# Performance work log

Hardware: AMD Instinct MI355X
Metric: run time of the kernel (lower is better)

## Reference

```python
import jax, jax.numpy as jnp
import numpy as np

# Sizes (must match input_specs)
N_CHR, E_CHR = 50000, 500000
N_SLV, E_SLV = 30000, 300000
B = 256            # number of graphs in the batch
FEAT = 64          # num_node_feats
DIM = 128          # hidden dim
HALF = DIM // 2    # last GCN layer output
ENS = 3            # ensemble per branch type


def setup_inputs() -> dict:
    key = jax.random.key(0)
    ks = jax.random.split(key, 20)
    g = lambda k, shape, fan_in: jax.random.normal(k, shape, dtype=jnp.float32) / np.sqrt(fan_in)
    inp = {
        'chr_x': jax.random.normal(ks[0], (N_CHR, FEAT), dtype=jnp.float32),
        'slv_x': jax.random.normal(ks[1], (N_SLV, FEAT), dtype=jnp.float32),
        'chr_edge_index': jax.random.randint(ks[2], (2, E_CHR), 0, N_CHR),
        'slv_edge_index': jax.random.randint(ks[3], (2, E_SLV), 0, N_SLV),
        'chr_x_batch': jnp.sort(jax.random.randint(ks[4], (N_CHR,), 0, B)),
        'slv_x_batch': jnp.sort(jax.random.randint(ks[5], (N_SLV,), 0, B)),
        # GCN weights, stacked over ensemble (GCNConv: bias=False)
        'chr_W0': g(ks[6], (ENS, FEAT, DIM), FEAT),
        'chr_W1': g(ks[7], (ENS, DIM, DIM), DIM),
        'chr_W2': g(ks[8], (ENS, DIM, HALF), DIM),
        'slv_W0': g(ks[9], (ENS, FEAT, DIM), FEAT),
        'slv_W1': g(ks[10], (ENS, DIM, DIM), DIM),
        'slv_W2': g(ks[11], (ENS, DIM, HALF), DIM),
        # per-ensemble projection heads (nn.Linear with bias)
        'cfc_W': g(ks[12], (ENS, HALF, DIM), HALF),
        'cfc_b': jnp.zeros((ENS, DIM), dtype=jnp.float32),
        'sfc_W': g(ks[13], (ENS, HALF, DIM), HALF),
        'sfc_b': jnp.zeros((ENS, DIM), dtype=jnp.float32),
        # final MLP head
        'fc1_W': g(ks[14], (2 * ENS * DIM, DIM), 2 * ENS * DIM),
        'fc1_b': jnp.zeros((DIM,), dtype=jnp.float32),
        'fc2_W': g(ks[15], (DIM, 1), DIM),
        'fc2_b': jnp.zeros((1,), dtype=jnp.float32),
    }
    return inp


def _gcn(x, W, src, dst, n_nodes):
    # GCNConv(normalize=False, bias=False, aggr='add'):
    # out[i] = sum_{(j,i) in E} (x @ W)[j]   (no self-loops, no normalization)
    h = x @ W
    return jax.ops.segment_sum(h[src], dst, num_segments=n_nodes)


def _branch(x, W0, W1, W2, edge_index, batch_ids, n_nodes):
    src, dst = edge_index[0], edge_index[1]
    h = jax.nn.relu(_gcn(x, W0, src, dst, n_nodes))
    h = jax.nn.relu(_gcn(h, W1, src, dst, n_nodes))
    h = jax.nn.relu(_gcn(h, W2, src, dst, n_nodes))
    # global_add_pool
    return jax.ops.segment_sum(h, batch_ids, num_segments=B)  # [B, HALF]


def reference(chr_x, slv_x, chr_W0, chr_W1, chr_W2, slv_W0, slv_W1, slv_W2,
              cfc_W, cfc_b, sfc_W, sfc_b, fc1_W, fc1_b, fc2_W, fc2_b,
              chr_edge_index, slv_edge_index, chr_x_batch, slv_x_batch):
    # vmap over the ensemble dimension (independent GCN stacks share inputs)
    rep_chr = jax.vmap(lambda w0, w1, w2: _branch(chr_x, w0, w1, w2, chr_edge_index, chr_x_batch, N_CHR))(
        chr_W0, chr_W1, chr_W2)  # [ENS, B, HALF]
    rep_slv = jax.vmap(lambda w0, w1, w2: _branch(slv_x, w0, w1, w2, slv_edge_index, slv_x_batch, N_SLV))(
        slv_W0, slv_W1, slv_W2)  # [ENS, B, HALF]
    ind_chr = jax.nn.relu(jnp.einsum('ebd,edh->ebh', rep_chr, cfc_W) + cfc_b[:, None, :])  # [ENS, B, DIM]
    ind_slv = jax.nn.relu(jnp.einsum('ebd,edh->ebh', rep_slv, sfc_W) + sfc_b[:, None, :])
    # torch.cat(ind_chr + ind_slv, dim=1): chr branches first, then slv branches
    hg = jnp.concatenate([
        jnp.transpose(ind_chr, (1, 0, 2)).reshape(B, ENS * DIM),
        jnp.transpose(ind_slv, (1, 0, 2)).reshape(B, ENS * DIM)], axis=1)  # [B, 2*ENS*DIM]
    hg = jax.nn.relu(hg @ fc1_W + fc1_b)
    out = hg @ fc2_W + fc2_b  # [B, 1]
    return out
```

## Files before the change

### kernel.cpp

```cpp
#include <hip/hip_runtime.h>

#define N_CHR 50000
#define E_CHR 500000
#define N_SLV 30000
#define E_SLV 300000
#define E_TOT (E_CHR + E_SLV)
#define BATCH_B 256
#define FEAT 64
#define DIM 128
#define HALF 64
#define ENSN 3
#define CB_CHR ((N_CHR + 255) / 256)
#define CB_SLV ((N_SLV + 255) / 256)
#define CB_TOT (CB_CHR + CB_SLV)
#define NBLK 128
#define SLOTS (NBLK * 4)
#define CHUNK ((E_TOT + NBLK - 1) / NBLK)

typedef unsigned int u32;
typedef unsigned short u16;
typedef __attribute__((ext_vector_type(8))) short short8;
typedef __attribute__((ext_vector_type(4))) float floatx4;
typedef __attribute__((ext_vector_type(4))) unsigned int u32x4;


__device__ inline u16 f2b(float f) {
    u32 u = __builtin_bit_cast(u32, f);
    u += 0x7FFFu + ((u >> 16) & 1u);
    return (u16)(u >> 16);
}
__device__ inline float b2f_lo(u32 v) { return __builtin_bit_cast(float, v << 16); }
__device__ inline float b2f_hi(u32 v) { return __builtin_bit_cast(float, v & 0xFFFF0000u); }
__device__ inline u32 packb(float a, float b) { return (u32)f2b(a) | ((u32)f2b(b) << 16); }

__device__ inline void acc8(float* a, u32x4 v) {
    a[0] += b2f_lo(v.x); a[1] += b2f_hi(v.x);
    a[2] += b2f_lo(v.y); a[3] += b2f_hi(v.y);
    a[4] += b2f_lo(v.z); a[5] += b2f_hi(v.z);
    a[6] += b2f_lo(v.w); a[7] += b2f_hi(v.w);
}


__global__ void xconv_k(const float* __restrict__ xc, const float* __restrict__ xs,
                        u16* __restrict__ oc, u16* __restrict__ os) {
    const int nc = N_CHR * FEAT, ns = N_SLV * FEAT;
    int i = blockIdx.x * blockDim.x + threadIdx.x;
    int stride = gridDim.x * blockDim.x;
    for (; i < nc + ns; i += stride) {
        if (i < nc) oc[i] = f2b(xc[i]);
        else os[i - nc] = f2b(xs[i - nc]);
    }
}


__global__ void wconv6_k(const float* __restrict__ cW0, const float* __restrict__ cW1,
                         const float* __restrict__ cW2, const float* __restrict__ sW0,
                         const float* __restrict__ sW1, const float* __restrict__ sW2,
                         u16* __restrict__ cW0t, u16* __restrict__ cW1t, u16* __restrict__ cW2t,
                         u16* __restrict__ sW0t, u16* __restrict__ sW1t, u16* __restrict__ sW2t) {
    int z = blockIdx.z, e = blockIdx.y;
    const float* W; u16* Wt; int K, N;
    switch (z) {
        case 0: W = cW0; Wt = cW0t; K = FEAT; N = DIM;  break;
        case 1: W = cW1; Wt = cW1t; K = DIM;  N = DIM;  break;
        case 2: W = cW2; Wt = cW2t; K = DIM;  N = HALF; break;
        case 3: W = sW0; Wt = sW0t; K = FEAT; N = DIM;  break;
        case 4: W = sW1; Wt = sW1t; K = DIM;  N = DIM;  break;
        default: W = sW2; Wt = sW2t; K = DIM; N = HALF; break;
    }
    int idx = blockIdx.x * 256 + threadIdx.x;
    if (idx >= K * N) return;
    int k = idx / N, nn = idx - k * N;
    Wt[((size_t)e * N + nn) * K + k] = f2b(W[(size_t)e * K * N + idx]);
}


__global__ __launch_bounds__(256) void hist_blocks_k(
        const int* __restrict__ cdst, const int* __restrict__ sdst,
        int* __restrict__ gh, int* __restrict__ btot) {
    __shared__ int h[4][CB_TOT];
    int blk = blockIdx.x, t = threadIdx.x, wv = t >> 6;
    for (int i = t; i < 4 * CB_TOT; i += 256) ((int*)h)[i] = 0;
    __syncthreads();
    int s = blk * CHUNK, e = s + CHUNK;
    if (e > E_TOT) e = E_TOT;
    for (int i = s + t; i < e; i += 256) {
        int bkt = (i < E_CHR) ? (cdst[i] >> 8) : (CB_CHR + (sdst[i - E_CHR] >> 8));
        atomicAdd(&h[wv][bkt], 1);
    }
    __syncthreads();
    for (int j = t; j < CB_TOT; j += 256) {
        int s0 = h[0][j], s1 = h[1][j], s2 = h[2][j], s3 = h[3][j];
        gh[j * SLOTS + blk * 4 + 0] = s0;
        gh[j * SLOTS + blk * 4 + 1] = s1;
        gh[j * SLOTS + blk * 4 + 2] = s2;
        gh[j * SLOTS + blk * 4 + 3] = s3;
        int tot = s0 + s1 + s2 + s3;
        if (tot) atomicAdd(&btot[j], tot);
    }
}

__global__ void coarse_scan_k(const int* __restrict__ cnt, int* __restrict__ off) {
    int t = threadIdx.x;
    const int PER = (CB_TOT + 63) / 64;
    int loc[PER];
    int sum = 0;
    int s = t * PER;
#pragma unroll
    for (int k = 0; k < PER; k++) {
        int i = s + k;
        int v = (i < CB_TOT) ? cnt[i] : 0;
        loc[k] = sum;
        sum += v;
    }
    int inc = sum;
#pragma unroll
    for (int o = 1; o < 64; o <<= 1) {
        int sh = __shfl_up(inc, o, 64);
        if (t >= o) inc += sh;
    }
    int pre = inc - sum;
#pragma unroll
    for (int k = 0; k < PER; k++) {
        int i = s + k;
        if (i < CB_TOT) off[i] = pre + loc[k];
    }
    if (t == 63) off[CB_TOT] = inc;
}

__device__ inline int block_exscan(int v) {
    int lane = threadIdx.x & 63, wv = threadIdx.x >> 6;
    int inc = v;
#pragma unroll
    for (int o = 1; o < 64; o <<= 1) {
        int t = __shfl_up(inc, o, 64);
        if (lane >= o) inc += t;
    }
    __shared__ int ws[4];
    if (lane == 63) ws[wv] = inc;
    __syncthreads();
    if (threadIdx.x == 0) {
        int c = 0;
#pragma unroll
        for (int k = 0; k < 4; k++) { int t = ws[k]; ws[k] = c; c += t; }
    }
    __syncthreads();
    int r = ws[wv] + inc - v;
    __syncthreads();
    return r;
}

__global__ __launch_bounds__(256) void block_base_k(int* __restrict__ gh,
                                                    const int* __restrict__ coff) {
    int j = blockIdx.x, t = threadIdx.x;
    int v0 = gh[j * SLOTS + 2 * t], v1 = gh[j * SLOTS + 2 * t + 1];
    int p = block_exscan(v0 + v1);
    gh[j * SLOTS + 2 * t] = coff[j] + p;
    gh[j * SLOTS + 2 * t + 1] = coff[j] + p + v0;
}

__global__ __launch_bounds__(256) void scatter2_k(
        const int* __restrict__ cei, const int* __restrict__ sei,
        const int* __restrict__ gh, u32* __restrict__ staging) {
    __shared__ int cur[4][CB_TOT];
    int blk = blockIdx.x, t = threadIdx.x, wv = t >> 6;
    for (int i = t; i < 4 * CB_TOT; i += 256) {
        int w = i / CB_TOT, j = i - w * CB_TOT;
        ((int*)cur)[i] = gh[j * SLOTS + blk * 4 + w];
    }
    __syncthreads();
    int s = blk * CHUNK, e = s + CHUNK;
    if (e > E_TOT) e = E_TOT;
    for (int i = s + t; i < e; i += 256) {
        int src, dst, bkt;
        if (i < E_CHR) {
            src = cei[i]; dst = cei[E_CHR + i]; bkt = dst >> 8;
        } else {
            int j2 = i - E_CHR;
            src = sei[j2]; dst = sei[E_SLV + j2]; bkt = CB_CHR + (dst >> 8);
        }
        int p = atomicAdd(&cur[wv][bkt], 1);
        staging[p] = (u32)src | ((u32)(dst & 255) << 17);
    }
}

__global__ __launch_bounds__(256) void bucket_sort_k(
        const u32* __restrict__ staging, const int* __restrict__ coff,
        int* __restrict__ off_c, int* __restrict__ off_s,
        int* __restrict__ csr_c, int* __restrict__ csr_s) {
    int b = blockIdx.x, t = threadIdx.x, wv = t >> 6;
    int isS = b >= CB_CHR;
    int base = coff[b], end = coff[b + 1];
    int n = isS ? N_SLV : N_CHR;
    int* off = isS ? off_s : off_c;
    int* csr = isS ? csr_s : csr_c;
    int outBase = isS ? base - E_CHR : base;
    int nodeBase = (isS ? (b - CB_CHR) : b) << 8;
    __shared__ int h4[4][256];
    __shared__ int cur[256];
    h4[0][t] = 0; h4[1][t] = 0; h4[2][t] = 0; h4[3][t] = 0;
    __syncthreads();
    for (int i = base + t; i < end; i += 256)
        atomicAdd(&h4[wv][staging[i] >> 17], 1);
    __syncthreads();
    int tot = h4[0][t] + h4[1][t] + h4[2][t] + h4[3][t];
    int p = block_exscan(tot);
    int node = nodeBase + t;
    if (node <= n) off[node] = outBase + p;
    cur[t] = p;
    __syncthreads();
    for (int i = base + t; i < end; i += 256) {
        u32 v = staging[i];
        int pos = atomicAdd(&cur[v >> 17], 1);
        csr[outBase + pos] = (int)(v & 0x1FFFFu);
    }
}


__global__ __launch_bounds__(256) void agg1gemm_k(
        const u16* __restrict__ Xc, const int* __restrict__ offc, const int* __restrict__ csrc,
        const u16* __restrict__ W0c, u16* __restrict__ Yc, int nc,
        const u16* __restrict__ Xs, const int* __restrict__ offs, const int* __restrict__ csrs,
        const u16* __restrict__ W0s, u16* __restrict__ Ys, int ns) {
    __shared__ u32x4 at4[64 * 8];
    __shared__ u32x4 wt4[128 * 8];
    int z = blockIdx.z;
    int n = z ? ns : nc;
    const int* off = z ? offs : offc;
    const int* csr = z ? csrs : csrc;
    const u32x4* X4 = (const u32x4*)(z ? Xs : Xc);
    const u16* W0 = z ? W0s : W0c;
    u16* Y = z ? Ys : Yc;
    int i0 = blockIdx.x * 64;
    if (i0 >= n) return;
    int t = threadIdx.x;
    int nl = t >> 2, c0 = t & 3;
    int i = i0 + nl;
    float a[16] = {0,0,0,0,0,0,0,0,0,0,0,0,0,0,0,0};
    if (i < n) {
        int s = off[i], e2 = off[i + 1], j = s;
        for (; j + 1 < e2; j += 2) {
            size_t r0 = (size_t)csr[j] * 8, r1 = (size_t)csr[j + 1] * 8;
            u32x4 v0 = X4[r0 + c0], v1 = X4[r0 + c0 + 4];
            u32x4 w0 = X4[r1 + c0], w1 = X4[r1 + c0 + 4];
            acc8(a, v0); acc8(a + 8, v1); acc8(a, w0); acc8(a + 8, w1);
        }
        if (j < e2) {
            size_t r0 = (size_t)csr[j] * 8;
            acc8(a, X4[r0 + c0]); acc8(a + 8, X4[r0 + c0 + 4]);
        }
    }
    u32x4 o0, o1;
    o0.x = packb(a[0], a[1]);  o0.y = packb(a[2], a[3]);
    o0.z = packb(a[4], a[5]);  o0.w = packb(a[6], a[7]);
    o1.x = packb(a[8], a[9]);  o1.y = packb(a[10], a[11]);
    o1.z = packb(a[12], a[13]); o1.w = packb(a[14], a[15]);
    int sw = nl & 7;
    at4[nl * 8 + (c0 ^ sw)] = o0;
    at4[nl * 8 + ((c0 + 4) ^ sw)] = o1;
    int wave = t >> 6, lane = t & 63, quad = lane >> 4, nq = lane & 15;
    int arow = wave * 16 + nq;
    for (int e = 0; e < ENSN; e++) {
        __syncthreads();
        const u16* We = W0 + (size_t)e * DIM * FEAT;
        for (int ci = t; ci < 128 * 8; ci += 256) {
            int row = ci >> 3, c = ci & 7;
            wt4[row * 8 + (c ^ (row & 7))] = *(const u32x4*)(We + (size_t)row * FEAT + c * 8);
        }
        __syncthreads();
        floatx4 acc[8];
#pragma unroll
        for (int tt = 0; tt < 8; tt++) acc[tt] = (floatx4)(0.f);
#pragma unroll
        for (int kt = 0; kt < 2; kt++) {
            int ck = kt * 4 + quad;
            short8 af = *(const short8*)&at4[arow * 8 + (ck ^ (arow & 7))];
#pragma unroll
            for (int tt = 0; tt < 8; tt++) {
                int br = tt * 16 + nq;
                short8 bf = *(const short8*)&wt4[br * 8 + (ck ^ (br & 7))];
                acc[tt] = __builtin_amdgcn_mfma_f32_16x16x32_bf16(af, bf, acc[tt], 0, 0, 0);
            }
        }
        u16* Ye = Y + (size_t)e * (size_t)n * DIM;
#pragma unroll
        for (int tt = 0; tt < 8; tt++)
#pragma unroll
            for (int r = 0; r < 4; r++) {
                int row = i0 + wave * 16 + quad * 4 + r;
                if (row < n) Ye[(size_t)row * DIM + tt * 16 + nq] = f2b(fmaxf(acc[tt][r], 0.f));
            }
    }
}


__global__ __launch_bounds__(256) void aggb128cs_k(
        const u16* __restrict__ Hc, const int* __restrict__ offc, const int* __restrict__ csrc,
        u16* __restrict__ Yc, int nc,
        const u16* __restrict__ Hs, const int* __restrict__ offs, const int* __restrict__ csrs,
        u16* __restrict__ Ys, int ns) {
    int z = blockIdx.z;
    int n = z ? ns : nc;
    const int* off = z ? offs : offc;
    const int* csr = z ? csrs : csrc;
    int e = blockIdx.y >> 1, ch = blockIdx.y & 1;
    const u32x4* He = (const u32x4*)((z ? Hs : Hc) + (size_t)e * n * DIM);
    u32x4* Ye = (u32x4*)((z ? Ys : Yc) + (size_t)e * n * DIM);
    int i = blockIdx.x * 32 + (threadIdx.x >> 3);
    if (i >= n) return;
    int l8 = (threadIdx.x & 7) + ch * 8;
    int s = off[i], e2 = off[i + 1];
    float a[8] = {0.f, 0.f, 0.f, 0.f, 0.f, 0.f, 0.f, 0.f};
    int j = s;
    for (; j + 3 < e2; j += 4) {
        u32x4 v0 = He[(size_t)csr[j] * 16 + l8];
        u32x4 v1 = He[(size_t)csr[j + 1] * 16 + l8];
        u32x4 v2 = He[(size_t)csr[j + 2] * 16 + l8];
        u32x4 v3 = He[(size_t)csr[j + 3] * 16 + l8];
        acc8(a, v0); acc8(a, v1); acc8(a, v2); acc8(a, v3);
    }
    for (; j < e2; j++) acc8(a, He[(size_t)csr[j] * 16 + l8]);
    u32x4 o;
    o.x = packb(a[0], a[1]); o.y = packb(a[2], a[3]);
    o.z = packb(a[4], a[5]); o.w = packb(a[6], a[7]);
    Ye[(size_t)i * 16 + l8] = o;
}


__global__ __launch_bounds__(256) void gemm23_k(
        const u16* __restrict__ Xc, const u16* __restrict__ W1c, const u16* __restrict__ W2c,
        u16* __restrict__ Yc, int nc,
        const u16* __restrict__ Xs, const u16* __restrict__ W1s, const u16* __restrict__ W2s,
        u16* __restrict__ Ys, int ns) {
    __shared__ u16 wlds[DIM * DIM];
    __shared__ u16 hlds[4 * 32 * DIM];
    const int z = blockIdx.z, e = blockIdx.y;
    const int n = z ? ns : nc;
    const u16* Xe = (z ? Xs : Xc) + (size_t)e * (size_t)n * DIM;
    const u16* W1 = (z ? W1s : W1c) + (size_t)e * DIM * DIM;
    const u16* W2 = (z ? W2s : W2c) + (size_t)e * HALF * DIM;
    u16* Ye = (z ? Ys : Yc) + (size_t)e * (size_t)n * HALF;
    for (int c = threadIdx.x; c < DIM * (DIM / 8); c += 256) {
        int row = c >> 4, seg = c & 15;
        *(short8*)(wlds + row * DIM + ((seg ^ (row & 15)) << 3)) =
            *(const short8*)(W1 + (size_t)row * DIM + (seg << 3));
    }
    __syncthreads();
    int wave = threadIdx.x >> 6, lane = threadIdx.x & 63;
    int quad = lane >> 4, nq = lane & 15;
    int m0 = blockIdx.x * 128 + wave * 32;
    floatx4 acc[2][8];
#pragma unroll
    for (int rg = 0; rg < 2; rg++)
#pragma unroll
        for (int t = 0; t < 8; t++) acc[rg][t] = (floatx4)(0.f);
#pragma unroll
    for (int kt = 0; kt < 4; kt++) {
        int k0 = kt * 32 + quad * 8;
        short8 a[2];
#pragma unroll
        for (int rg = 0; rg < 2; rg++) {
            int row = m0 + rg * 16 + nq;
            int rc = row < n ? row : (n - 1);
            a[rg] = *(const short8*)(Xe + (size_t)rc * DIM + k0);
        }
#pragma unroll
        for (int t = 0; t < 8; t++) {
            int rb = t * 16 + nq;
            short8 b = *(const short8*)(wlds + rb * DIM + ((((kt << 2) + quad) ^ nq) << 3));
#pragma unroll
            for (int rg = 0; rg < 2; rg++)
                acc[rg][t] = __builtin_amdgcn_mfma_f32_16x16x32_bf16(a[rg], b, acc[rg][t], 0, 0, 0);
        }
    }
    u16* hw = hlds + wave * 32 * DIM;
#pragma unroll
    for (int rg = 0; rg < 2; rg++)
#pragma unroll
        for (int t = 0; t < 8; t++)
#pragma unroll
            for (int r = 0; r < 4; r++) {
                int rl = rg * 16 + quad * 4 + r;
                int col = t * 16 + nq;
                hw[rl * DIM + (((col >> 3) ^ (rl & 15)) << 3) + (col & 7)] =
                    f2b(fmaxf(acc[rg][t][r], 0.f));
            }
    __syncthreads();
    for (int c = threadIdx.x; c < HALF * (DIM / 8); c += 256) {
        int row = c >> 4, seg = c & 15;
        *(short8*)(wlds + row * DIM + ((seg ^ (row & 15)) << 3)) =
            *(const short8*)(W2 + (size_t)row * DIM + (seg << 3));
    }
    __syncthreads();
    floatx4 acc2[2][4];
#pragma unroll
    for (int rg = 0; rg < 2; rg++)
#pragma unroll
        for (int t = 0; t < 4; t++) acc2[rg][t] = (floatx4)(0.f);
#pragma unroll
    for (int kt = 0; kt < 4; kt++) {
        int k0q = (kt << 2) + quad;
        short8 a[2];
#pragma unroll
        for (int rg = 0; rg < 2; rg++) {
            int rl = rg * 16 + nq;
            a[rg] = *(const short8*)(hw + rl * DIM + ((k0q ^ (rl & 15)) << 3));
        }
#pragma unroll
        for (int t = 0; t < 4; t++) {
            int rb = t * 16 + nq;
            short8 b = *(const short8*)(wlds + rb * DIM + ((k0q ^ nq) << 3));
#pragma unroll
            for (int rg = 0; rg < 2; rg++)
                acc2[rg][t] = __builtin_amdgcn_mfma_f32_16x16x32_bf16(a[rg], b, acc2[rg][t], 0, 0, 0);
        }
    }
#pragma unroll
    for (int rg = 0; rg < 2; rg++)
#pragma unroll
        for (int t = 0; t < 4; t++)
#pragma unroll
            for (int r = 0; r < 4; r++) {
                int row = m0 + rg * 16 + quad * 4 + r;
                if (row < n) Ye[(size_t)row * HALF + t * 16 + nq] = f2b(acc2[rg][t][r]);
            }
}


__global__ __launch_bounds__(256) void agg64poole_k(
        const u16* __restrict__ Pc, const int* __restrict__ offc, const int* __restrict__ csrc,
        const int* __restrict__ batc, int nc,
        const u16* __restrict__ Ps, const int* __restrict__ offs, const int* __restrict__ csrs,
        const int* __restrict__ bats, int ns,
        float* __restrict__ rep) {
    int z = blockIdx.z;
    int n = z ? ns : nc;
    const int* off = z ? offs : offc;
    const int* csr = z ? csrs : csrc;
    const int* batch = z ? bats : batc;
    const u16* P = z ? Ps : Pc;
    const u32x4* P0 = (const u32x4*)P;
    const u32x4* P1 = (const u32x4*)(P + (size_t)n * HALF);
    const u32x4* P2 = (const u32x4*)(P + 2 * (size_t)n * HALF);
    int i0 = blockIdx.x * 32;
    int nl = threadIdx.x >> 3, l8 = threadIdx.x & 7;
    int i = i0 + nl;
    float a0[8] = {0,0,0,0,0,0,0,0}, a1[8] = {0,0,0,0,0,0,0,0}, a2[8] = {0,0,0,0,0,0,0,0};
    if (i < n) {
        int s = off[i], e2 = off[i + 1];
        int j = s;
        for (; j + 1 < e2; j += 2) {
            size_t r0 = (size_t)csr[j] * 8 + l8, r1 = (size_t)csr[j + 1] * 8 + l8;
            u32x4 p0 = P0[r0], p1 = P1[r0], p2 = P2[r0];
            u32x4 q0 = P0[r1], q1 = P1[r1], q2 = P2[r1];
            acc8(a0, p0); acc8(a1, p1); acc8(a2, p2);
            acc8(a0, q0); acc8(a1, q1); acc8(a2, q2);
        }
        if (j < e2) {
            size_t r0 = (size_t)csr[j] * 8 + l8;
            acc8(a0, P0[r0]); acc8(a1, P1[r0]); acc8(a2, P2[r0]);
        }
    }
    __shared__ float sm[ENSN][32][64];
    __shared__ int gb[32];
#pragma unroll
    for (int k = 0; k < 8; k++) {
        sm[0][nl][l8 * 8 + k] = fmaxf(a0[k], 0.f);
        sm[1][nl][l8 * 8 + k] = fmaxf(a1[k], 0.f);
        sm[2][nl][l8 * 8 + k] = fmaxf(a2[k], 0.f);
    }
    if (threadIdx.x < 32) gb[threadIdx.x] = (i0 + (int)threadIdx.x < n) ? batch[i0 + threadIdx.x] : -1;
    __syncthreads();
    if (threadIdx.x < 192) {
        int e = threadIdx.x >> 6, f = threadIdx.x & 63;
        int colbase = z * (ENSN * HALF) + e * HALF + f;
        float acc = 0.f;
        int g = -2;
        for (int k = 0; k < 32; k++) {
            int gg = gb[k];
            if (gg != g) {
                if (g >= 0) atomicAdd(&rep[g * (2 * ENSN * HALF) + colbase], acc);
                acc = 0.f;
                g = gg;
            }
            if (gg >= 0) acc += sm[e][k][f];
        }
        if (g >= 0) atomicAdd(&rep[g * (2 * ENSN * HALF) + colbase], acc);
    }
}


__global__ __launch_bounds__(256) void headfinal_k(
        const float* __restrict__ rep,
        const float* __restrict__ cW, const float* __restrict__ cB,
        const float* __restrict__ sW, const float* __restrict__ sB,
        const float* __restrict__ W1, const float* __restrict__ b1,
        const float* __restrict__ W2, const float* __restrict__ b2,
        float* __restrict__ out) {
    int b = blockIdx.x, t = threadIdx.x;
    __shared__ float r[2 * ENSN * HALF];
    __shared__ float hg[2 * ENSN * DIM];
    __shared__ float red[DIM];
    for (int i = t; i < 2 * ENSN * HALF; i += 256) r[i] = rep[b * (2 * ENSN * HALF) + i];
    __syncthreads();
    for (int o = t; o < 2 * ENSN * DIM; o += 256) {
        int head = o >> 7, c = o & 127;
        int branch = head / ENSN, e = head - branch * ENSN;
        const float* W = (branch ? sW : cW) + (size_t)e * HALF * DIM;
        const float* rr = r + branch * (ENSN * HALF) + e * HALF;
        float acc = (branch ? sB : cB)[e * DIM + c];
#pragma unroll
        for (int k = 0; k < HALF; k++) acc = fmaf(rr[k], W[k * DIM + c], acc);
        hg[o] = fmaxf(acc, 0.f);
    }
    __syncthreads();
    if (t < DIM) {
        float acc = b1[t];
        for (int k = 0; k < 2 * ENSN * DIM; k++) acc = fmaf(hg[k], W1[k * DIM + t], acc);
        red[t] = fmaxf(acc, 0.f) * W2[t];
    }
    __syncthreads();
    if (t < 64) {
        float v = red[t] + red[t + 64];
#pragma unroll
        for (int o = 32; o > 0; o >>= 1) v += __shfl_down(v, o, 64);
        if (t == 0) out[b] = v + b2[0];
    }
}


extern "C" void kernel_launch(void* const* d_in, const int* in_sizes, int n_in,
                              void* d_out, int out_size, void* d_ws, size_t ws_size,
                              hipStream_t stream) {
    const float* chr_x = (const float*)d_in[0];
    const float* slv_x = (const float*)d_in[1];
    const int* chr_ei = (const int*)d_in[2];
    const int* slv_ei = (const int*)d_in[3];
    const int* chr_batch = (const int*)d_in[4];
    const int* slv_batch = (const int*)d_in[5];
    const float* chr_W0 = (const float*)d_in[6];
    const float* chr_W1 = (const float*)d_in[7];
    const float* chr_W2 = (const float*)d_in[8];
    const float* slv_W0 = (const float*)d_in[9];
    const float* slv_W1 = (const float*)d_in[10];
    const float* slv_W2 = (const float*)d_in[11];
    const float* cfc_W = (const float*)d_in[12];
    const float* cfc_b = (const float*)d_in[13];
    const float* sfc_W = (const float*)d_in[14];
    const float* sfc_b = (const float*)d_in[15];
    const float* fc1_W = (const float*)d_in[16];
    const float* fc1_b = (const float*)d_in[17];
    const float* fc2_W = (const float*)d_in[18];
    const float* fc2_b = (const float*)d_in[19];
    float* out = (float*)d_out;

    char* w = (char*)d_ws;
    auto carve = [&](size_t bytes) {
        void* p = (void*)w;
        w += (bytes + 255) & ~(size_t)255;
        return p;
    };
    int* off_chr = (int*)carve((N_CHR + 1) * sizeof(int));
    int* csr_chr = (int*)carve((size_t)E_CHR * sizeof(int));
    int* off_slv = (int*)carve((N_SLV + 1) * sizeof(int));
    int* csr_slv = (int*)carve((size_t)E_SLV * sizeof(int));
    int* btot    = (int*)carve(CB_TOT * sizeof(int));
    int* coff    = (int*)carve((CB_TOT + 1) * sizeof(int));
    int* gh      = (int*)carve((size_t)CB_TOT * SLOTS * sizeof(int));
    u32* staging = (u32*)carve((size_t)E_TOT * sizeof(u32));
    u16* cW0t = (u16*)carve((size_t)ENSN * DIM * FEAT * sizeof(u16));
    u16* cW1t = (u16*)carve((size_t)ENSN * DIM * DIM * sizeof(u16));
    u16* cW2t = (u16*)carve((size_t)ENSN * HALF * DIM * sizeof(u16));
    u16* sW0t = (u16*)carve((size_t)ENSN * DIM * FEAT * sizeof(u16));
    u16* sW1t = (u16*)carve((size_t)ENSN * DIM * DIM * sizeof(u16));
    u16* sW2t = (u16*)carve((size_t)ENSN * HALF * DIM * sizeof(u16));
    u16* xb_chr = (u16*)carve((size_t)N_CHR * FEAT * sizeof(u16));
    u16* xb_slv = (u16*)carve((size_t)N_SLV * FEAT * sizeof(u16));
    float* rep = (float*)carve((size_t)BATCH_B * 2 * ENSN * HALF * sizeof(float));
    u16* bufP_c = (u16*)carve((size_t)ENSN * N_CHR * DIM * sizeof(u16));
    u16* bufQ_c = (u16*)carve((size_t)ENSN * N_CHR * DIM * sizeof(u16));
    u16* bufP_s = (u16*)carve((size_t)ENSN * N_SLV * DIM * sizeof(u16));
    u16* bufQ_s = (u16*)carve((size_t)ENSN * N_SLV * DIM * sizeof(u16));

    xconv_k<<<512, 256, 0, stream>>>(chr_x, slv_x, xb_chr, xb_slv);
    wconv6_k<<<dim3(64, ENSN, 6), 256, 0, stream>>>(chr_W0, chr_W1, chr_W2,
                                                    slv_W0, slv_W1, slv_W2,
                                                    cW0t, cW1t, cW2t, sW0t, sW1t, sW2t);

    hipMemsetAsync(btot, 0, CB_TOT * sizeof(int), stream);
    hist_blocks_k<<<NBLK, 256, 0, stream>>>(chr_ei + E_CHR, slv_ei + E_SLV, gh, btot);
    coarse_scan_k<<<1, 64, 0, stream>>>(btot, coff);
    block_base_k<<<CB_TOT, 256, 0, stream>>>(gh, coff);
    scatter2_k<<<NBLK, 256, 0, stream>>>(chr_ei, slv_ei, gh, staging);
    bucket_sort_k<<<CB_TOT, 256, 0, stream>>>(staging, coff, off_chr, off_slv, csr_chr, csr_slv);

    hipMemsetAsync(rep, 0, (size_t)BATCH_B * 2 * ENSN * HALF * sizeof(float), stream);

    agg1gemm_k<<<dim3((N_CHR + 63) / 64, 1, 2), 256, 0, stream>>>(
        xb_chr, off_chr, csr_chr, cW0t, bufP_c, N_CHR,
        xb_slv, off_slv, csr_slv, sW0t, bufP_s, N_SLV);
    aggb128cs_k<<<dim3((N_CHR + 31) / 32, ENSN * 2, 2), 256, 0, stream>>>(
        bufP_c, off_chr, csr_chr, bufQ_c, N_CHR,
        bufP_s, off_slv, csr_slv, bufQ_s, N_SLV);
    gemm23_k<<<dim3((N_CHR + 127) / 128, ENSN, 2), 256, 0, stream>>>(
        bufQ_c, cW1t, cW2t, bufP_c, N_CHR,
        bufQ_s, sW1t, sW2t, bufP_s, N_SLV);
    agg64poole_k<<<dim3((N_CHR + 31) / 32, 1, 2), 256, 0, stream>>>(
        bufP_c, off_chr, csr_chr, chr_batch, N_CHR,
        bufP_s, off_slv, csr_slv, slv_batch, N_SLV, rep);

    headfinal_k<<<BATCH_B, 256, 0, stream>>>(rep, cfc_W, cfc_b, sfc_W, sfc_b,
                                             fc1_W, fc1_b, fc2_W, fc2_b, out);
}
```

Before: 373.5 us.

## Fuse layer-2 aggregation into GEMM23, fold memsets into kernels, split pool by ensemble

The layer-2 neighbor aggregation now runs inside the GEMM kernel. Each lane gathers and accumulates its rows' neighbor features into registers, and those registers become the MFMA A operands. This removes the write and re-read of the aggregated buffer and one launch. The two memsets move into existing kernels (xconv zeroes btot, hist zeroes rep), and the layer-3 pool kernel gains a grid dimension over the ensemble so each block handles one ensemble member. The costs are higher register pressure, less parallelism in the gather phase of the fused kernel, and the csr/off indices being read once per ensemble in the pool kernel.

```diff
diff --git a/kernel.cpp b/kernel.cpp
--- a/kernel.cpp
+++ b/kernel.cpp
@@ -16,6 +16,7 @@
 #define NBLK 128
 #define SLOTS (NBLK * 4)
 #define CHUNK ((E_TOT + NBLK - 1) / NBLK)
+#define REP_SZ (BATCH_B * 2 * ENSN * HALF)
 
 typedef unsigned int u32;
 typedef unsigned short u16;
@@ -42,7 +43,9 @@
 
 
 __global__ void xconv_k(const float* __restrict__ xc, const float* __restrict__ xs,
-                        u16* __restrict__ oc, u16* __restrict__ os) {
+                        u16* __restrict__ oc, u16* __restrict__ os, int* __restrict__ btot) {
+    if (blockIdx.x == 0)
+        for (int i = threadIdx.x; i < CB_TOT; i += 256) btot[i] = 0;
     const int nc = N_CHR * FEAT, ns = N_SLV * FEAT;
     int i = blockIdx.x * blockDim.x + threadIdx.x;
     int stride = gridDim.x * blockDim.x;
@@ -77,7 +80,8 @@
 
 __global__ __launch_bounds__(256) void hist_blocks_k(
         const int* __restrict__ cdst, const int* __restrict__ sdst,
-        int* __restrict__ gh, int* __restrict__ btot) {
+        int* __restrict__ gh, int* __restrict__ btot, float* __restrict__ rep) {
+    for (int i = blockIdx.x * 256 + threadIdx.x; i < REP_SZ; i += NBLK * 256) rep[i] = 0.f;
     __shared__ int h[4][CB_TOT];
     int blk = blockIdx.x, t = threadIdx.x, wv = t >> 6;
     for (int i = t; i < 4 * CB_TOT; i += 256) ((int*)h)[i] = 0;
@@ -294,49 +298,18 @@
 }
 
 
-__global__ __launch_bounds__(256) void aggb128cs_k(
+__global__ __launch_bounds__(256) void agg2gemm23_k(
         const u16* __restrict__ Hc, const int* __restrict__ offc, const int* __restrict__ csrc,
-        u16* __restrict__ Yc, int nc,
+        const u16* __restrict__ W1c, const u16* __restrict__ W2c, u16* __restrict__ Yc, int nc,
         const u16* __restrict__ Hs, const int* __restrict__ offs, const int* __restrict__ csrs,
-        u16* __restrict__ Ys, int ns) {
-    int z = blockIdx.z;
-    int n = z ? ns : nc;
-    const int* off = z ? offs : offc;
-    const int* csr = z ? csrs : csrc;
-    int e = blockIdx.y >> 1, ch = blockIdx.y & 1;
-    const u32x4* He = (const u32x4*)((z ? Hs : Hc) + (size_t)e * n * DIM);
-    u32x4* Ye = (u32x4*)((z ? Ys : Yc) + (size_t)e * n * DIM);
-    int i = blockIdx.x * 32 + (threadIdx.x >> 3);
-    if (i >= n) return;
-    int l8 = (threadIdx.x & 7) + ch * 8;
-    int s = off[i], e2 = off[i + 1];
-    float a[8] = {0.f, 0.f, 0.f, 0.f, 0.f, 0.f, 0.f, 0.f};
-    int j = s;
-    for (; j + 3 < e2; j += 4) {
-        u32x4 v0 = He[(size_t)csr[j] * 16 + l8];
-        u32x4 v1 = He[(size_t)csr[j + 1] * 16 + l8];
-        u32x4 v2 = He[(size_t)csr[j + 2] * 16 + l8];
-        u32x4 v3 = He[(size_t)csr[j + 3] * 16 + l8];
-        acc8(a, v0); acc8(a, v1); acc8(a, v2); acc8(a, v3);
-    }
-    for (; j < e2; j++) acc8(a, He[(size_t)csr[j] * 16 + l8]);
-    u32x4 o;
-    o.x = packb(a[0], a[1]); o.y = packb(a[2], a[3]);
-    o.z = packb(a[4], a[5]); o.w = packb(a[6], a[7]);
-    Ye[(size_t)i * 16 + l8] = o;
-}
-
-
-__global__ __launch_bounds__(256) void gemm23_k(
-        const u16* __restrict__ Xc, const u16* __restrict__ W1c, const u16* __restrict__ W2c,
-        u16* __restrict__ Yc, int nc,
-        const u16* __restrict__ Xs, const u16* __restrict__ W1s, const u16* __restrict__ W2s,
-        u16* __restrict__ Ys, int ns) {
+        const u16* __restrict__ W1s, const u16* __restrict__ W2s, u16* __restrict__ Ys, int ns) {
     __shared__ u16 wlds[DIM * DIM];
     __shared__ u16 hlds[4 * 32 * DIM];
     const int z = blockIdx.z, e = blockIdx.y;
     const int n = z ? ns : nc;
-    const u16* Xe = (z ? Xs : Xc) + (size_t)e * (size_t)n * DIM;
+    const int* off = z ? offs : offc;
+    const int* csr = z ? csrs : csrc;
+    const u32x4* He = (const u32x4*)((z ? Hs : Hc) + (size_t)e * (size_t)n * DIM);
     const u16* W1 = (z ? W1s : W1c) + (size_t)e * DIM * DIM;
     const u16* W2 = (z ? W2s : W2c) + (size_t)e * HALF * DIM;
     u16* Ye = (z ? Ys : Yc) + (size_t)e * (size_t)n * HALF;
@@ -345,10 +318,38 @@
         *(short8*)(wlds + row * DIM + ((seg ^ (row & 15)) << 3)) =
             *(const short8*)(W1 + (size_t)row * DIM + (seg << 3));
     }
-    __syncthreads();
     int wave = threadIdx.x >> 6, lane = threadIdx.x & 63;
     int quad = lane >> 4, nq = lane & 15;
     int m0 = blockIdx.x * 128 + wave * 32;
+    float ag[2][4][8];
+#pragma unroll
+    for (int rg = 0; rg < 2; rg++)
+#pragma unroll
+        for (int kt = 0; kt < 4; kt++)
+#pragma unroll
+            for (int k = 0; k < 8; k++) ag[rg][kt][k] = 0.f;
+#pragma unroll
+    for (int rg = 0; rg < 2; rg++) {
+        int r = m0 + rg * 16 + nq;
+        if (r < n) {
+            int s = off[r], e2 = off[r + 1], j = s;
+            for (; j + 1 < e2; j += 2) {
+                size_t b0 = (size_t)csr[j] * 16 + quad, b1 = (size_t)csr[j + 1] * 16 + quad;
+                u32x4 v0 = He[b0], v1 = He[b0 + 4], v2 = He[b0 + 8], v3 = He[b0 + 12];
+                u32x4 w0 = He[b1], w1 = He[b1 + 4], w2 = He[b1 + 8], w3 = He[b1 + 12];
+                acc8(ag[rg][0], v0); acc8(ag[rg][1], v1);
+                acc8(ag[rg][2], v2); acc8(ag[rg][3], v3);
+                acc8(ag[rg][0], w0); acc8(ag[rg][1], w1);
+                acc8(ag[rg][2], w2); acc8(ag[rg][3], w3);
+            }
+            if (j < e2) {
+                size_t b0 = (size_t)csr[j] * 16 + quad;
+                acc8(ag[rg][0], He[b0]);     acc8(ag[rg][1], He[b0 + 4]);
+                acc8(ag[rg][2], He[b0 + 8]); acc8(ag[rg][3], He[b0 + 12]);
+            }
+        }
+    }
+    __syncthreads();
     floatx4 acc[2][8];
 #pragma unroll
     for (int rg = 0; rg < 2; rg++)
@@ -356,13 +357,15 @@
         for (int t = 0; t < 8; t++) acc[rg][t] = (floatx4)(0.f);
 #pragma unroll
     for (int kt = 0; kt < 4; kt++) {
-        int k0 = kt * 32 + quad * 8;
         short8 a[2];
 #pragma unroll
         for (int rg = 0; rg < 2; rg++) {
-            int row = m0 + rg * 16 + nq;
-            int rc = row < n ? row : (n - 1);
-            a[rg] = *(const short8*)(Xe + (size_t)rc * DIM + k0);
+            u32x4 t4;
+            t4.x = packb(ag[rg][kt][0], ag[rg][kt][1]);
+            t4.y = packb(ag[rg][kt][2], ag[rg][kt][3]);
+            t4.z = packb(ag[rg][kt][4], ag[rg][kt][5]);
+            t4.w = packb(ag[rg][kt][6], ag[rg][kt][7]);
+            a[rg] = __builtin_bit_cast(short8, t4);
         }
 #pragma unroll
         for (int t = 0; t < 8; t++) {
@@ -427,52 +430,41 @@
 }
 
 
-__global__ __launch_bounds__(256) void agg64poole_k(
+__global__ __launch_bounds__(256) void agg3pool_k(
         const u16* __restrict__ Pc, const int* __restrict__ offc, const int* __restrict__ csrc,
         const int* __restrict__ batc, int nc,
         const u16* __restrict__ Ps, const int* __restrict__ offs, const int* __restrict__ csrs,
         const int* __restrict__ bats, int ns,
         float* __restrict__ rep) {
-    int z = blockIdx.z;
+    int z = blockIdx.z, e = blockIdx.y;
     int n = z ? ns : nc;
     const int* off = z ? offs : offc;
     const int* csr = z ? csrs : csrc;
     const int* batch = z ? bats : batc;
-    const u16* P = z ? Ps : Pc;
-    const u32x4* P0 = (const u32x4*)P;
-    const u32x4* P1 = (const u32x4*)(P + (size_t)n * HALF);
-    const u32x4* P2 = (const u32x4*)(P + 2 * (size_t)n * HALF);
+    const u32x4* Pe = (const u32x4*)((z ? Ps : Pc) + (size_t)e * (size_t)n * HALF);
     int i0 = blockIdx.x * 32;
     int nl = threadIdx.x >> 3, l8 = threadIdx.x & 7;
     int i = i0 + nl;
-    float a0[8] = {0,0,0,0,0,0,0,0}, a1[8] = {0,0,0,0,0,0,0,0}, a2[8] = {0,0,0,0,0,0,0,0};
+    float a[8] = {0,0,0,0,0,0,0,0};
     if (i < n) {
-        int s = off[i], e2 = off[i + 1];
-        int j = s;
-        for (; j + 1 < e2; j += 2) {
-            size_t r0 = (size_t)csr[j] * 8 + l8, r1 = (size_t)csr[j + 1] * 8 + l8;
-            u32x4 p0 = P0[r0], p1 = P1[r0], p2 = P2[r0];
-            u32x4 q0 = P0[r1], q1 = P1[r1], q2 = P2[r1];
-            acc8(a0, p0); acc8(a1, p1); acc8(a2, p2);
-            acc8(a0, q0); acc8(a1, q1); acc8(a2, q2);
-        }
-        if (j < e2) {
-            size_t r0 = (size_t)csr[j] * 8 + l8;
-            acc8(a0, P0[r0]); acc8(a1, P1[r0]); acc8(a2, P2[r0]);
-        }
-    }
-    __shared__ float sm[ENSN][32][64];
+        int s = off[i], e2 = off[i + 1], j = s;
+        for (; j + 3 < e2; j += 4) {
+            u32x4 v0 = Pe[(size_t)csr[j] * 8 + l8];
+            u32x4 v1 = Pe[(size_t)csr[j + 1] * 8 + l8];
+            u32x4 v2 = Pe[(size_t)csr[j + 2] * 8 + l8];
+            u32x4 v3 = Pe[(size_t)csr[j + 3] * 8 + l8];
+            acc8(a, v0); acc8(a, v1); acc8(a, v2); acc8(a, v3);
+        }
+        for (; j < e2; j++) acc8(a, Pe[(size_t)csr[j] * 8 + l8]);
+    }
+    __shared__ float sm[32][64];
     __shared__ int gb[32];
 #pragma unroll
-    for (int k = 0; k < 8; k++) {
-        sm[0][nl][l8 * 8 + k] = fmaxf(a0[k], 0.f);
-        sm[1][nl][l8 * 8 + k] = fmaxf(a1[k], 0.f);
-        sm[2][nl][l8 * 8 + k] = fmaxf(a2[k], 0.f);
-    }
+    for (int k = 0; k < 8; k++) sm[nl][l8 * 8 + k] = fmaxf(a[k], 0.f);
     if (threadIdx.x < 32) gb[threadIdx.x] = (i0 + (int)threadIdx.x < n) ? batch[i0 + threadIdx.x] : -1;
     __syncthreads();
-    if (threadIdx.x < 192) {
-        int e = threadIdx.x >> 6, f = threadIdx.x & 63;
+    if (threadIdx.x < 64) {
+        int f = threadIdx.x;
         int colbase = z * (ENSN * HALF) + e * HALF + f;
         float acc = 0.f;
         int g = -2;
@@ -483,7 +475,7 @@
                 acc = 0.f;
                 g = gg;
             }
-            if (gg >= 0) acc += sm[e][k][f];
+            if (gg >= 0) acc += sm[k][f];
         }
         if (g >= 0) atomicAdd(&rep[g * (2 * ENSN * HALF) + colbase], acc);
     }
@@ -576,38 +568,32 @@
     u16* sW2t = (u16*)carve((size_t)ENSN * HALF * DIM * sizeof(u16));
     u16* xb_chr = (u16*)carve((size_t)N_CHR * FEAT * sizeof(u16));
     u16* xb_slv = (u16*)carve((size_t)N_SLV * FEAT * sizeof(u16));
-    float* rep = (float*)carve((size_t)BATCH_B * 2 * ENSN * HALF * sizeof(float));
+    float* rep = (float*)carve((size_t)REP_SZ * sizeof(float));
     u16* bufP_c = (u16*)carve((size_t)ENSN * N_CHR * DIM * sizeof(u16));
     u16* bufQ_c = (u16*)carve((size_t)ENSN * N_CHR * DIM * sizeof(u16));
     u16* bufP_s = (u16*)carve((size_t)ENSN * N_SLV * DIM * sizeof(u16));
     u16* bufQ_s = (u16*)carve((size_t)ENSN * N_SLV * DIM * sizeof(u16));
 
-    xconv_k<<<512, 256, 0, stream>>>(chr_x, slv_x, xb_chr, xb_slv);
+    xconv_k<<<512, 256, 0, stream>>>(chr_x, slv_x, xb_chr, xb_slv, btot);
     wconv6_k<<<dim3(64, ENSN, 6), 256, 0, stream>>>(chr_W0, chr_W1, chr_W2,
                                                     slv_W0, slv_W1, slv_W2,
                                                     cW0t, cW1t, cW2t, sW0t, sW1t, sW2t);
 
-    hipMemsetAsync(btot, 0, CB_TOT * sizeof(int), stream);
-    hist_blocks_k<<<NBLK, 256, 0, stream>>>(chr_ei + E_CHR, slv_ei + E_SLV, gh, btot);
+    hist_blocks_k<<<NBLK, 256, 0, stream>>>(chr_ei + E_CHR, slv_ei + E_SLV, gh, btot, rep);
     coarse_scan_k<<<1, 64, 0, stream>>>(btot, coff);
     block_base_k<<<CB_TOT, 256, 0, stream>>>(gh, coff);
     scatter2_k<<<NBLK, 256, 0, stream>>>(chr_ei, slv_ei, gh, staging);
     bucket_sort_k<<<CB_TOT, 256, 0, stream>>>(staging, coff, off_chr, off_slv, csr_chr, csr_slv);
 
-    hipMemsetAsync(rep, 0, (size_t)BATCH_B * 2 * ENSN * HALF * sizeof(float), stream);
-
     agg1gemm_k<<<dim3((N_CHR + 63) / 64, 1, 2), 256, 0, stream>>>(
         xb_chr, off_chr, csr_chr, cW0t, bufP_c, N_CHR,
         xb_slv, off_slv, csr_slv, sW0t, bufP_s, N_SLV);
-    aggb128cs_k<<<dim3((N_CHR + 31) / 32, ENSN * 2, 2), 256, 0, stream>>>(
-        bufP_c, off_chr, csr_chr, bufQ_c, N_CHR,
-        bufP_s, off_slv, csr_slv, bufQ_s, N_SLV);
-    gemm23_k<<<dim3((N_CHR + 127) / 128, ENSN, 2), 256, 0, stream>>>(
-        bufQ_c, cW1t, cW2t, bufP_c, N_CHR,
-        bufQ_s, sW1t, sW2t, bufP_s, N_SLV);
-    agg64poole_k<<<dim3((N_CHR + 31) / 32, 1, 2), 256, 0, stream>>>(
-        bufP_c, off_chr, csr_chr, chr_batch, N_CHR,
-        bufP_s, off_slv, csr_slv, slv_batch, N_SLV, rep);
+    agg2gemm23_k<<<dim3((N_CHR + 127) / 128, ENSN, 2), 256, 0, stream>>>(
+        bufP_c, off_chr, csr_chr, cW1t, cW2t, bufQ_c, N_CHR,
+        bufP_s, off_slv, csr_slv, sW1t, sW2t, bufQ_s, N_SLV);
+    agg3pool_k<<<dim3((N_CHR + 31) / 32, ENSN, 2), 256, 0, stream>>>(
+        bufQ_c, off_chr, csr_chr, chr_batch, N_CHR,
+        bufQ_s, off_slv, csr_slv, slv_batch, N_SLV, rep);
 
     headfinal_k<<<BATCH_B, 256, 0, stream>>>(rep, cfc_W, cfc_b, sfc_W, sfc_b,
                                              fc1_W, fc1_b, fc2_W, fc2_b, out);
```

Result: slower. 408.4 us (+9.4%).
